# Kernel optimization log

Measured on AMD Instinct MI355X. Metric: run time of the kernel, lower is better.

Reference implementation:

```python
import jax, jax.numpy as jnp
import numpy as np

B, N_OBJ, N_VAL, E, H, HEADS = 512, 10, 200, 420, 128, 4
NPG = 1 + N_OBJ + N_VAL  # nodes per graph = 211
N = B * NPG
FMIN = float(np.finfo(np.float32).min)


def _gat_conv(x, src, dst, W, att_src, att_dst, bias, concat):
    # PyG GATConv (v1): linear (no bias) -> per-head attention logits ->
    # leaky_relu(a_src[j]+a_dst[i]) -> softmax over edges grouped by dst -> scatter-sum
    heads = att_src.shape[0]
    xs = (x @ W).reshape(N, heads, -1)            # [N, heads, C]
    a_src = (xs * att_src).sum(-1)                # [N, heads]
    a_dst = (xs * att_dst).sum(-1)                # [N, heads]
    alpha = jax.nn.leaky_relu(a_src[src] + a_dst[dst], 0.2)   # [Etot, heads]
    amax = jax.ops.segment_max(alpha, dst, num_segments=N)
    ex = jnp.exp(alpha - amax[dst])
    denom = jax.ops.segment_sum(ex, dst, num_segments=N)
    alpha = ex / (denom[dst] + 1e-16)
    out = jax.ops.segment_sum(xs[src] * alpha[..., None], dst, num_segments=N)  # [N,heads,C]
    out = out.reshape(N, -1) if concat else out.mean(axis=1)
    return out + bias


def setup_inputs() -> dict:
    key = jax.random.key(0)
    ks = jax.random.split(key, 24)
    s = 0.1
    C1 = H // HEADS  # 32
    inp = {
        'head_node': jax.random.normal(ks[0], (B, 2), jnp.float32),
        'objective_nodes': jax.random.normal(ks[1], (B, N_OBJ, 2), jnp.float32),
        'value_nodes': jax.random.normal(ks[2], (B, N_VAL, 5), jnp.float32),
        'edge_indices': jax.random.randint(ks[3], (B, 2, E), 0, NPG, jnp.int64 if jax.config.jax_enable_x64 else jnp.int32),
        'accept_mask': jnp.ones((B, 2), jnp.float32),
        'W_head': jax.random.normal(ks[4], (2, H)) * s, 'b_head': jnp.zeros((H,)),
        'W_obj': jax.random.normal(ks[5], (2, H)) * s, 'b_obj': jnp.zeros((H,)),
        'W_val': jax.random.normal(ks[6], (5, H)) * s, 'b_val': jnp.zeros((H,)),
        'W1': jax.random.normal(ks[7], (H, HEADS * C1)) * s,
        'att_src1': jax.random.normal(ks[8], (HEADS, C1)) * s,
        'att_dst1': jax.random.normal(ks[9], (HEADS, C1)) * s,
        'b1': jnp.zeros((HEADS * C1,)),
        'W2': jax.random.normal(ks[10], (H, HEADS * H)) * s,
        'att_src2': jax.random.normal(ks[11], (HEADS, H)) * s,
        'att_dst2': jax.random.normal(ks[12], (HEADS, H)) * s,
        'b2': jnp.zeros((H,)),
        'W_acc': jax.random.normal(ks[13], (H, 2)) * 0.01, 'b_acc': jnp.zeros((2,)),
        'W_off': jax.random.normal(ks[14], (H, 1)) * 0.01, 'b_off': jnp.zeros((1,)),
        'W_vf': jax.random.normal(ks[15], (H, 1)) * s, 'b_vf': jnp.zeros((1,)),
    }
    return inp


def reference(head_node, objective_nodes, value_nodes, edge_indices, accept_mask,
              W_head, b_head, W_obj, b_obj, W_val, b_val,
              W1, att_src1, att_dst1, b1, W2, att_src2, att_dst2, b2,
              W_acc, b_acc, W_off, b_off, W_vf, b_vf):
    # node encoders + ReLU
    h_head = jax.nn.relu(head_node @ W_head + b_head)                  # [B,H]
    h_obj = jax.nn.relu(objective_nodes @ W_obj + b_obj)               # [B,N_OBJ,H]
    h_val = jax.nn.relu(value_nodes @ W_val + b_val)                   # [B,N_VAL,H]
    h_nodes = jnp.concatenate([h_head[:, None], h_obj, h_val], axis=1)  # [B,NPG,H]
    x = h_nodes.reshape(N, H)
    # batch graphs: offset per-graph edge indices, add self loops
    offs = (jnp.arange(B, dtype=edge_indices.dtype) * NPG)[:, None, None]
    ei = (edge_indices + offs).transpose(1, 0, 2).reshape(2, -1)       # [2, B*E]
    loops = jnp.arange(N, dtype=edge_indices.dtype)
    src = jnp.concatenate([ei[0], loops])
    dst = jnp.concatenate([ei[1], loops])
    # GAT: layer1 concat heads, ReLU (BasicGNN inter-layer act), layer2 mean heads
    x1 = jax.nn.relu(_gat_conv(x, src, dst, W1, att_src1, att_dst1, b1, True))
    x2 = _gat_conv(x1, src, dst, W2, att_src2, att_dst2, b2, False)
    h_out = jax.nn.relu(x2).reshape(B, NPG, H)
    h_head_out = h_out[:, 0]                                           # [B,H]
    h_val_out = h_out[:, -N_VAL:]                                      # [B,N_VAL,H]
    offer_logits = (h_val_out @ W_off + b_off).squeeze(-1)             # [B,N_VAL]
    accept_inf_mask = jnp.maximum(jnp.log(accept_mask), FMIN)
    accept_logits = h_head_out @ W_acc + b_acc + accept_inf_mask       # [B,2]
    vf = h_head_out @ W_vf + b_vf                                      # [B,1]
    return jnp.concatenate([accept_logits, offer_logits, vf], axis=-1)  # [B, 2+N_VAL+1]
```

## Files before the change

### kernel.cpp

```cpp
#include <hip/hip_runtime.h>

typedef unsigned short u16;
typedef unsigned int u32;
typedef short short8 __attribute__((ext_vector_type(8)));
typedef float f32x4 __attribute__((ext_vector_type(4)));

#define NB   512
#define NPG  211
#define NOBJ 10
#define NVAL 200
#define NE   420
#define NN   (NB * NPG)

__device__ __forceinline__ float bf2f(u16 u){
  union { unsigned i; float f; } v; v.i = ((unsigned)u) << 16; return v.f;
}
__device__ __forceinline__ u16 f2bf(float f){
  union { float f; unsigned i; } v; v.f = f;
  return (u16)((v.i + 0x7FFFu + ((v.i >> 16) & 1u)) >> 16);
}
__device__ __forceinline__ float lo_bf(u32 u){ union{u32 i;float f;}v; v.i=u<<16; return v.f; }
__device__ __forceinline__ float hi_bf(u32 u){ union{u32 i;float f;}v; v.i=u&0xffff0000u; return v.f; }
__device__ __forceinline__ u32 pack_bf(float a, float b){ return (u32)f2bf(a) | ((u32)f2bf(b)<<16); }
__device__ __forceinline__ float lrelu(float s){ return s > 0.f ? s : 0.2f * s; }
__device__ __forceinline__ short8 pack8(ushort4 a, ushort4 b){
  short8 v;
  v[0]=(short)a.x; v[1]=(short)a.y; v[2]=(short)a.z; v[3]=(short)a.w;
  v[4]=(short)b.x; v[5]=(short)b.y; v[6]=(short)b.z; v[7]=(short)b.w;
  return v;
}
__device__ __forceinline__ int swz(int r, int c){
  return (r << 7) + (((c & ~3) ^ ((r & 15) << 2)) | (c & 3));
}
__device__ __forceinline__ int s16(int r, int c){
  return (r << 7) + ((((c >> 3) ^ (r & 15)) << 3) | (c & 7));
}

#define AS_GLOBAL(p) ((const __attribute__((address_space(1))) void*)((const void*)(p)))
#define AS_LDS(p)    ((__attribute__((address_space(3))) void*)((void*)(p)))

__global__ __launch_bounds__(256) void k_prept(const float* __restrict__ W1, const float* __restrict__ W2,
                                               u16* __restrict__ W1t, u16* __restrict__ W2t){
  int gid = blockIdx.x * 256 + threadIdx.x;
  if (gid < 16384){
    int k = gid >> 7, n = gid & 127;
    W1t[n * 128 + k] = f2bf(W1[k * 128 + n]);
  } else {
    int t = gid - 16384;
    int n = t >> 9, kk = t & 511;
    int h = kk >> 7, c = kk & 127;
    W2t[n * 512 + kk] = f2bf(W2[c * 512 + h * 128 + n]);
  }
}

__global__ __launch_bounds__(256) void k_prepwm(const float* __restrict__ W2, const float* __restrict__ as2,
                                                const float* __restrict__ ad2,
                                                float* __restrict__ wms, float* __restrict__ wmd){
  int gid = blockIdx.x * 256 + threadIdx.x;
  int which = gid >> 9, hk = gid & 511;
  int h = hk >> 7, k = hk & 127;
  const float* av = which ? ad2 : as2;
  float s = 0.f;
  for (int j = 0; j < 128; ++j)
    s += W2[k * 512 + h * 128 + j] * av[h * 128 + j];
  (which ? wmd : wms)[hk] = s;
}


__global__ __launch_bounds__(256) void k_embed2(
    const float* __restrict__ head, const float* __restrict__ obj, const float* __restrict__ val,
    const float* __restrict__ Wh, const float* __restrict__ bh,
    const float* __restrict__ Wo, const float* __restrict__ bo,
    const float* __restrict__ Wv, const float* __restrict__ bv,
    u16* __restrict__ x){
  int gid = blockIdx.x * 256 + threadIdx.x;
  int n = gid >> 5, cc = (gid & 31) << 2;
  int g = n / NPG, loc = n - g * NPG;
  float a[4];
  if (loc == 0){
    const float* in = head + (size_t)g * 2;
    float i0 = in[0], i1 = in[1];
    #pragma unroll
    for (int t = 0; t < 4; ++t){ int c = cc + t; a[t] = bh[c] + i0 * Wh[c] + i1 * Wh[128 + c]; }
  } else if (loc <= NOBJ){
    const float* in = obj + ((size_t)g * NOBJ + (loc - 1)) * 2;
    float i0 = in[0], i1 = in[1];
    #pragma unroll
    for (int t = 0; t < 4; ++t){ int c = cc + t; a[t] = bo[c] + i0 * Wo[c] + i1 * Wo[128 + c]; }
  } else {
    const float* in = val + ((size_t)g * NVAL + (loc - 11)) * 5;
    float f[5];
    #pragma unroll
    for (int k = 0; k < 5; ++k) f[k] = in[k];
    #pragma unroll
    for (int t = 0; t < 4; ++t){
      int c = cc + t; float s = bv[c];
      #pragma unroll
      for (int k = 0; k < 5; ++k) s += f[k] * Wv[k * 128 + c];
      a[t] = s;
    }
  }
  ushort4 u;
  u.x = f2bf(fmaxf(a[0], 0.f)); u.y = f2bf(fmaxf(a[1], 0.f));
  u.z = f2bf(fmaxf(a[2], 0.f)); u.w = f2bf(fmaxf(a[3], 0.f));
  *(ushort4*)&x[(size_t)n * 128 + cc] = u;
}

__global__ __launch_bounds__(256) void k_csr2(const int* __restrict__ eidx,
                                              int* __restrict__ coff, int* __restrict__ csrc){
  __shared__ int sEs[420], sEd[420], sTmp[256], sOff[212], sSrc[632];
  int g = blockIdx.x, tid = threadIdx.x;
  const int4* e4 = (const int4*)(eidx + (size_t)g * 840);
  for (int i = tid; i < 105; i += 256){ ((int4*)sEs)[i] = e4[i]; ((int4*)sEd)[i] = e4[105 + i]; }
  __syncthreads();
  int deg = 0;
  if (tid < NPG){
    deg = 1;
    const int4* p4 = (const int4*)sEd;
    #pragma unroll 4
    for (int i = 0; i < 105; ++i){
      int4 v = p4[i];
      deg += (v.x == tid) + (v.y == tid) + (v.z == tid) + (v.w == tid);
    }
  }
  int v = deg;
  #pragma unroll
  for (int st = 1; st < 256; st <<= 1){
    sTmp[tid] = v;
    __syncthreads();
    if (tid >= st) v += sTmp[tid - st];
    __syncthreads();
  }
  if (tid < NPG) sOff[tid] = v - deg;
  if (tid == NPG - 1) sOff[NPG] = v;
  __syncthreads();
  if (tid < NPG){
    int p = sOff[tid];
    sSrc[p++] = tid;
    const int4* pd4 = (const int4*)sEd;
    const int4* ps4 = (const int4*)sEs;
    for (int i = 0; i < 105; ++i){
      int4 d = pd4[i]; int4 s = ps4[i];
      if (d.x == tid) sSrc[p++] = s.x;
      if (d.y == tid) sSrc[p++] = s.y;
      if (d.z == tid) sSrc[p++] = s.z;
      if (d.w == tid) sSrc[p++] = s.w;
    }
  }
  __syncthreads();
  if (tid < 212) coff[(size_t)g * 212 + tid] = sOff[tid];
  for (int i = tid; i < 631; i += 256) csrc[(size_t)g * 632 + i] = sSrc[i];
}

template<int KCH, bool RELU>
__global__ __launch_bounds__(512) void k_mm(const u16* __restrict__ A, size_t chunkStride,
                                            const u16* __restrict__ Bt, int bstride,
                                            const float* __restrict__ bias, u16* __restrict__ C){
  __shared__ u16 sA[128 * 128];
  __shared__ u16 sB[128 * 128];
  const int tid = threadIdx.x, lane = tid & 63, w = tid >> 6;
  const int l15 = lane & 15, lg = lane >> 4;
  const int row0 = blockIdx.x * 128;
  f32x4 acc[8];
  #pragma unroll
  for (int ni = 0; ni < 8; ++ni) acc[ni] = (f32x4){0,0,0,0};

  #pragma unroll 1
  for (int ch = 0; ch < KCH; ++ch){
    const u16* Ab = A + (size_t)ch * chunkStride + (size_t)row0 * 128;
    const u16* Bb = Bt + ch * 128;
    #pragma unroll
    for (int i = 0; i < 4; ++i){
      int r = w * 16 + i * 4 + (lane >> 4);
      int c16 = lane & 15;
      int sw = (c16 ^ (r & 15)) << 4;
      __builtin_amdgcn_global_load_lds(AS_GLOBAL((const char*)(Ab + (size_t)r * 128) + sw),
                                       AS_LDS(&sA[(w * 16 + i * 4) * 128]), 16, 0, 0);
      __builtin_amdgcn_global_load_lds(AS_GLOBAL((const char*)(Bb + (size_t)r * bstride) + sw),
                                       AS_LDS(&sB[(w * 16 + i * 4) * 128]), 16, 0, 0);
    }
    __syncthreads();
    #pragma unroll
    for (int kk = 0; kk < 4; ++kk){
      int k0 = kk * 32 + lg * 4;
      int rr = w * 16 + l15;
      short8 af = pack8(*(const ushort4*)&sA[s16(rr, k0)],
                        *(const ushort4*)&sA[s16(rr, k0 + 16)]);
      #pragma unroll
      for (int ni = 0; ni < 8; ++ni){
        int cc = ni * 16 + l15;
        short8 bf = pack8(*(const ushort4*)&sB[s16(cc, k0)],
                          *(const ushort4*)&sB[s16(cc, k0 + 16)]);
        acc[ni] = __builtin_amdgcn_mfma_f32_16x16x32_bf16(af, bf, acc[ni], 0, 0, 0);
      }
    }
    __syncthreads();
  }
  const int r0 = row0 + w * 16 + lg * 4;
  #pragma unroll
  for (int ni = 0; ni < 8; ++ni){
    int col = ni * 16 + l15;
    float bv = RELU ? bias[col] : 0.f;
    #pragma unroll
    for (int r = 0; r < 4; ++r){
      float v = acc[ni][r];
      if (RELU) v = fmaxf(v + bv, 0.f);
      C[(size_t)(r0 + r) * 128 + col] = f2bf(v);
    }
  }
}

__global__ __launch_bounds__(256) void k_att1k(const u16* __restrict__ xs1,
                                               const float* __restrict__ as1, const float* __restrict__ ad1,
                                               float* __restrict__ Ls, float* __restrict__ Ld){
  int t = blockIdx.x * 256 + threadIdx.x;
  int n = t >> 2, h = t & 3;
  const u16* xr = xs1 + (size_t)n * 128 + h * 32;
  float s = 0.f, d = 0.f;
  #pragma unroll
  for (int j = 0; j < 8; ++j){
    ushort4 xv = *(const ushort4*)(xr + j * 4);
    #pragma unroll
    for (int q = 0; q < 4; ++q){
      float xf = bf2f(((const u16*)&xv)[q]);
      int c = h * 32 + j * 4 + q;
      s += xf * as1[c];
      d += xf * ad1[c];
    }
  }
  Ls[t] = s; Ld[t] = d;
}

__global__ __launch_bounds__(256) void k_att2k(const u16* __restrict__ x1,
                                               const float* __restrict__ wms, const float* __restrict__ wmd,
                                               float* __restrict__ Ls, float* __restrict__ Ld){
  __shared__ float sw[1024];
  int tid = threadIdx.x;
  for (int i = tid; i < 512; i += 256) sw[i] = wms[i];
  for (int i = tid; i < 512; i += 256) sw[512 + i] = wmd[i];
  __syncthreads();
  int t = blockIdx.x * 256 + tid;
  int n = t >> 2, h = t & 3;
  const u16* xr = x1 + (size_t)n * 128;
  const float* wsp = sw + h * 128;
  const float* wdp = sw + 512 + h * 128;
  float s = 0.f, d = 0.f;
  #pragma unroll
  for (int j = 0; j < 32; ++j){
    ushort4 xv = *(const ushort4*)(xr + j * 4);
    #pragma unroll
    for (int q = 0; q < 4; ++q){
      float xf = bf2f(((const u16*)&xv)[q]);
      s += xf * wsp[j * 4 + q];
      d += xf * wdp[j * 4 + q];
    }
  }
  Ls[t] = s; Ld[t] = d;
}

__global__ __launch_bounds__(256) void k_smk(const float* __restrict__ Ls, const float* __restrict__ Ld,
                                             const int* __restrict__ coff, const int* __restrict__ csrc,
                                             float* __restrict__ wn, float* __restrict__ rden, float fold){
  int g = blockIdx.x >> 2;
  int t = ((blockIdx.x & 3) << 8) + threadIdx.x;
  if (t >= NPG * 4) return;
  int dst = t >> 2, h = t & 3;
  int gb = g * NPG;
  int o0 = coff[(size_t)g * 212 + dst], o1 = coff[(size_t)g * 212 + dst + 1];
  const int* sp = csrc + (size_t)g * 632;
  float ad = Ld[(size_t)(gb + dst) * 4 + h];
  float m = -3e38f;
  for (int e = o0; e < o1; ++e) m = fmaxf(m, lrelu(Ls[(size_t)(gb + sp[e]) * 4 + h] + ad));
  float dn = 0.f;
  float* wp = wn + (size_t)g * 2528 + h * 632;
  for (int e = o0; e < o1; ++e){
    float ee = __expf(lrelu(Ls[(size_t)(gb + sp[e]) * 4 + h] + ad) - m);
    wp[e] = ee; dn += ee;
  }
  rden[(size_t)(gb + dst) * 4 + h] = fold / (dn + 1e-16f);
}

__global__ __launch_bounds__(256) void k_gat1k(const u16* __restrict__ xs1,
                                               const float* __restrict__ wn, const float* __restrict__ rden,
                                               const int* __restrict__ coff, const int* __restrict__ csrc,
                                               const float* __restrict__ b1, u16* __restrict__ x1){
  int bid = blockIdx.x;
  int g = bid / 53, ch = bid - g * 53;
  int dst = ch * 4 + (threadIdx.x >> 6);
  if (dst >= NPG) return;
  int lane = threadIdx.x & 63;
  int cp = lane << 1, hh = lane >> 4;
  int gb = g * NPG;
  int o0 = coff[(size_t)g * 212 + dst], o1 = coff[(size_t)g * 212 + dst + 1];
  const int* sp = csrc + (size_t)g * 632;
  const float* wp = wn + (size_t)g * 2528 + hh * 632;
  float a0 = 0.f, a1 = 0.f;
  for (int e = o0; e < o1; ++e){
    int src = sp[e];
    u32 f = *(const u32*)&xs1[(size_t)(gb + src) * 128 + cp];
    float w = wp[e];
    a0 += w * lo_bf(f); a1 += w * hi_bf(f);
  }
  float rv = rden[(size_t)(gb + dst) * 4 + hh];
  *(u32*)&x1[(size_t)(gb + dst) * 128 + cp] =
    pack_bf(fmaxf(a0 * rv + b1[cp], 0.f), fmaxf(a1 * rv + b1[cp + 1], 0.f));
}

__global__ __launch_bounds__(256) void k_gat2k(const u16* __restrict__ x1,
                                               const float* __restrict__ wn, const float* __restrict__ rden,
                                               const int* __restrict__ coff, const int* __restrict__ csrc,
                                               u16* __restrict__ y){
  int bid = blockIdx.x;
  int g = bid / 53, ch = bid - g * 53;
  int dst = ch * 4 + (threadIdx.x >> 6);
  if (dst >= NPG) return;
  int lane = threadIdx.x & 63;
  int cp = lane << 1;
  int gb = g * NPG;
  int o0 = coff[(size_t)g * 212 + dst], o1 = coff[(size_t)g * 212 + dst + 1];
  const int* sp = csrc + (size_t)g * 632;
  const float* wb = wn + (size_t)g * 2528;
  float a0[4] = {0,0,0,0}, a1[4] = {0,0,0,0};
  for (int e = o0; e < o1; ++e){
    int src = sp[e];
    u32 f = *(const u32*)&x1[(size_t)(gb + src) * 128 + cp];
    float xl = lo_bf(f), xh = hi_bf(f);
    #pragma unroll
    for (int h = 0; h < 4; ++h){
      float w = wb[h * 632 + e];
      a0[h] += w * xl; a1[h] += w * xh;
    }
  }
  #pragma unroll
  for (int h = 0; h < 4; ++h){
    float rv = rden[(size_t)(gb + dst) * 4 + h];
    *(u32*)&y[(size_t)h * NN * 128 + (size_t)(gb + dst) * 128 + cp] =
      pack_bf(a0[h] * rv, a1[h] * rv);
  }
}

__global__ __launch_bounds__(256) void k_final2(const u16* __restrict__ out2, const float* __restrict__ amask,
                                                const float* __restrict__ Wacc, const float* __restrict__ bacc,
                                                const float* __restrict__ Woff, const float* __restrict__ boff,
                                                const float* __restrict__ Wvf,  const float* __restrict__ bvf,
                                                float* __restrict__ out){
  int g = blockIdx.x >> 2;
  int t = ((blockIdx.x & 3) << 8) + threadIdx.x;
  if (t >= 812) return;
  int o = t >> 2, q = t & 3;
  float s = 0.f;
  if (o < 200){
    const u16* row = out2 + (size_t)(g * NPG + 11 + o) * 128;
    #pragma unroll
    for (int j = 0; j < 8; ++j){
      int c = q * 32 + j * 4;
      ushort4 xv = *(const ushort4*)(row + c);
      s += bf2f(xv.x)*Woff[c] + bf2f(xv.y)*Woff[c+1] + bf2f(xv.z)*Woff[c+2] + bf2f(xv.w)*Woff[c+3];
    }
  } else if (o < 202){
    int j2 = o - 200;
    const u16* row = out2 + (size_t)(g * NPG) * 128;
    #pragma unroll
    for (int j = 0; j < 8; ++j){
      int c = q * 32 + j * 4;
      ushort4 xv = *(const ushort4*)(row + c);
      s += bf2f(xv.x)*Wacc[c*2+j2] + bf2f(xv.y)*Wacc[(c+1)*2+j2]
         + bf2f(xv.z)*Wacc[(c+2)*2+j2] + bf2f(xv.w)*Wacc[(c+3)*2+j2];
    }
  } else {
    const u16* row = out2 + (size_t)(g * NPG) * 128;
    #pragma unroll
    for (int j = 0; j < 8; ++j){
      int c = q * 32 + j * 4;
      ushort4 xv = *(const ushort4*)(row + c);
      s += bf2f(xv.x)*Wvf[c] + bf2f(xv.y)*Wvf[c+1] + bf2f(xv.z)*Wvf[c+2] + bf2f(xv.w)*Wvf[c+3];
    }
  }
  s += __shfl_xor(s, 1);
  s += __shfl_xor(s, 2);
  if (q == 0){
    if (o < 200){
      out[(size_t)g * 203 + 2 + o] = s + boff[0];
    } else if (o < 202){
      int j2 = o - 200;
      float lm = logf(amask[g * 2 + j2]);
      out[(size_t)g * 203 + j2] = s + bacc[j2] + fmaxf(lm, -3.402823466e38f);
    } else {
      out[(size_t)g * 203 + 202] = s + bvf[0];
    }
  }
}

extern "C" void kernel_launch(void* const* d_in, const int* in_sizes, int n_in,
                              void* d_out, int out_size, void* d_ws, size_t ws_size,
                              hipStream_t stream){
  (void)in_sizes; (void)n_in; (void)out_size; (void)ws_size;
  const float* head = (const float*)d_in[0];
  const float* obj  = (const float*)d_in[1];
  const float* val  = (const float*)d_in[2];
  const int*   eidx = (const int*)d_in[3];
  const float* amask= (const float*)d_in[4];
  const float* Wh   = (const float*)d_in[5];
  const float* bh   = (const float*)d_in[6];
  const float* Wo   = (const float*)d_in[7];
  const float* bo   = (const float*)d_in[8];
  const float* Wv   = (const float*)d_in[9];
  const float* bv   = (const float*)d_in[10];
  const float* W1   = (const float*)d_in[11];
  const float* as1  = (const float*)d_in[12];
  const float* ad1  = (const float*)d_in[13];
  const float* b1   = (const float*)d_in[14];
  const float* W2   = (const float*)d_in[15];
  const float* as2  = (const float*)d_in[16];
  const float* ad2  = (const float*)d_in[17];
  const float* b2   = (const float*)d_in[18];
  const float* Wacc = (const float*)d_in[19];
  const float* bacc = (const float*)d_in[20];
  const float* Woff = (const float*)d_in[21];
  const float* boff = (const float*)d_in[22];
  const float* Wvf  = (const float*)d_in[23];
  const float* bvf  = (const float*)d_in[24];
  float* out = (float*)d_out;

  char* ws = (char*)d_ws;
  u16*   W1t = (u16*)ws;
  u16*   W2t = (u16*)(ws + 32768);
  float* wms = (float*)(ws + 163840);
  float* wmd = (float*)(ws + 165888);

  k_prept<<<320, 256, 0, stream>>>(W1, W2, W1t, W2t);
  k_prepwm<<<4, 256, 0, stream>>>(W2, as2, ad2, wms, wmd);

  int*   coff = (int*)(ws + 167936);
  int*   csrc = (int*)(ws + 602112);
  float* aLs  = (float*)(ws + 1896448);
  float* aLd  = (float*)(ws + 3624960);
  float* wn   = (float*)(ws + 5353472);
  float* rden = (float*)(ws + 10530816);
  u16*   x    = (u16*)(ws + 12259328);
  u16*   xs1  = (u16*)(ws + 39915520);
  u16*   y    = (u16*)(ws + 67571712);

  k_embed2<<<NN * 32 / 256, 256, 0, stream>>>(head, obj, val, Wh, bh, Wo, bo, Wv, bv, x);
  k_csr2<<<NB, 256, 0, stream>>>(eidx, coff, csrc);
  k_mm<1, false><<<NN / 128, 512, 0, stream>>>(x, 0, W1t, 128, nullptr, xs1);
  k_att1k<<<NN * 4 / 256, 256, 0, stream>>>(xs1, as1, ad1, aLs, aLd);
  k_smk<<<NB * 4, 256, 0, stream>>>(aLs, aLd, coff, csrc, wn, rden, 1.0f);
  k_gat1k<<<NB * 53, 256, 0, stream>>>(xs1, wn, rden, coff, csrc, b1, x);
  k_att2k<<<NN * 4 / 256, 256, 0, stream>>>(x, wms, wmd, aLs, aLd);
  k_smk<<<NB * 4, 256, 0, stream>>>(aLs, aLd, coff, csrc, wn, rden, 0.25f);
  k_gat2k<<<NB * 53, 256, 0, stream>>>(x, wn, rden, coff, csrc, y);
  k_mm<4, true><<<NN / 128, 512, 0, stream>>>(y, (size_t)NN * 128, W2t, 512, b2, xs1);
  k_final2<<<NB * 4, 256, 0, stream>>>(xs1, amask, Wacc, bacc, Woff, boff, Wvf, bvf, out);
}
```

Before: 272.6 us.

## Fuse layer-2 aggregation, W2 matmul and output heads into one per-graph kernel

Replaces the separate layer-2 aggregation kernel, the 4-head MFMA matmul and the final head kernel with one kernel that runs one 512-thread block per graph. The block stages the graph's x1 rows, attention weights and CSR data in LDS, aggregates each head into LDS, feeds it to bf16 MFMA against W2, then applies bias, ReLU and the output projections from LDS. This removes the large intermediate y tensor and the out2 round trip through global memory, along with two launches. In exchange it uses about 122KB of LDS per block, which allows only one block per CU, so there are 512 blocks and little latency hiding.

```diff
diff --git a/kernel.cpp b/kernel.cpp
--- a/kernel.cpp
+++ b/kernel.cpp
@@ -306,87 +306,163 @@
     pack_bf(fmaxf(a0 * rv + b1[cp], 0.f), fmaxf(a1 * rv + b1[cp + 1], 0.f));
 }
 
-__global__ __launch_bounds__(256) void k_gat2k(const u16* __restrict__ x1,
-                                               const float* __restrict__ wn, const float* __restrict__ rden,
-                                               const int* __restrict__ coff, const int* __restrict__ csrc,
-                                               u16* __restrict__ y){
-  int bid = blockIdx.x;
-  int g = bid / 53, ch = bid - g * 53;
-  int dst = ch * 4 + (threadIdx.x >> 6);
-  if (dst >= NPG) return;
-  int lane = threadIdx.x & 63;
-  int cp = lane << 1;
-  int gb = g * NPG;
-  int o0 = coff[(size_t)g * 212 + dst], o1 = coff[(size_t)g * 212 + dst + 1];
-  const int* sp = csrc + (size_t)g * 632;
-  const float* wb = wn + (size_t)g * 2528;
-  float a0[4] = {0,0,0,0}, a1[4] = {0,0,0,0};
-  for (int e = o0; e < o1; ++e){
-    int src = sp[e];
-    u32 f = *(const u32*)&x1[(size_t)(gb + src) * 128 + cp];
-    float xl = lo_bf(f), xh = hi_bf(f);
-    #pragma unroll
-    for (int h = 0; h < 4; ++h){
-      float w = wb[h * 632 + e];
-      a0[h] += w * xl; a1[h] += w * xh;
-    }
-  }
-  #pragma unroll
+__global__ __launch_bounds__(512) void k_gg2(
+    const u16* __restrict__ x1, const float* __restrict__ wn, const float* __restrict__ rden,
+    const int* __restrict__ coff, const int* __restrict__ csrc,
+    const u16* __restrict__ W2t, const float* __restrict__ b2,
+    const float* __restrict__ amask,
+    const float* __restrict__ Wacc, const float* __restrict__ bacc,
+    const float* __restrict__ Woff, const float* __restrict__ boff,
+    const float* __restrict__ Wvf,  const float* __restrict__ bvf,
+    float* __restrict__ out)
+{
+  __shared__ __align__(16) char sm[124896];
+  u16*   sX1  = (u16*)sm;
+  u16*   sY   = (u16*)(sm + 54016);
+  float* sW   = (float*)(sm + 108032);
+  float* sDen = (float*)(sm + 118144);
+  int*   sOff = (int*)(sm + 121520);
+  int*   sSrc = (int*)(sm + 122368);
+
+  const int g = blockIdx.x, tid = threadIdx.x;
+  const int lane = tid & 63, w = tid >> 6;
+  const int l15 = lane & 15, lg = lane >> 4;
+  const int cp = lane << 1;
+
+  {
+    const uint4* src = (const uint4*)(x1 + (size_t)g * NPG * 128);
+    uint4* dst = (uint4*)sX1;
+    for (int i = tid; i < 3376; i += 512) dst[i] = src[i];
+    const float* wsrc = wn + (size_t)g * 2528;
+    for (int i = tid; i < 2528; i += 512) sW[i] = wsrc[i];
+    const float* rsrc = rden + (size_t)g * 844;
+    for (int i = tid; i < 844; i += 512) sDen[i] = rsrc[i];
+    for (int i = tid; i < 212; i += 512) sOff[i] = coff[(size_t)g * 212 + i];
+    const int* ssrc = csrc + (size_t)g * 632;
+    for (int i = tid; i < 632; i += 512) sSrc[i] = ssrc[i];
+  }
+  __syncthreads();
+
+  f32x4 acc[2][8];
+  #pragma unroll
+  for (int m = 0; m < 2; ++m)
+    #pragma unroll
+    for (int ni = 0; ni < 8; ++ni) acc[m][ni] = (f32x4){0,0,0,0};
+  const int rt0 = w, rt1 = w + 8;
+  const bool has1 = (rt1 < 14);
+
+  #pragma unroll 1
   for (int h = 0; h < 4; ++h){
-    float rv = rden[(size_t)(gb + dst) * 4 + h];
-    *(u32*)&y[(size_t)h * NN * 128 + (size_t)(gb + dst) * 128 + cp] =
-      pack_bf(a0[h] * rv, a1[h] * rv);
-  }
-}
-
-__global__ __launch_bounds__(256) void k_final2(const u16* __restrict__ out2, const float* __restrict__ amask,
-                                                const float* __restrict__ Wacc, const float* __restrict__ bacc,
-                                                const float* __restrict__ Woff, const float* __restrict__ boff,
-                                                const float* __restrict__ Wvf,  const float* __restrict__ bvf,
-                                                float* __restrict__ out){
-  int g = blockIdx.x >> 2;
-  int t = ((blockIdx.x & 3) << 8) + threadIdx.x;
-  if (t >= 812) return;
-  int o = t >> 2, q = t & 3;
-  float s = 0.f;
-  if (o < 200){
-    const u16* row = out2 + (size_t)(g * NPG + 11 + o) * 128;
-    #pragma unroll
-    for (int j = 0; j < 8; ++j){
-      int c = q * 32 + j * 4;
-      ushort4 xv = *(const ushort4*)(row + c);
-      s += bf2f(xv.x)*Woff[c] + bf2f(xv.y)*Woff[c+1] + bf2f(xv.z)*Woff[c+2] + bf2f(xv.w)*Woff[c+3];
-    }
-  } else if (o < 202){
-    int j2 = o - 200;
-    const u16* row = out2 + (size_t)(g * NPG) * 128;
-    #pragma unroll
-    for (int j = 0; j < 8; ++j){
-      int c = q * 32 + j * 4;
-      ushort4 xv = *(const ushort4*)(row + c);
-      s += bf2f(xv.x)*Wacc[c*2+j2] + bf2f(xv.y)*Wacc[(c+1)*2+j2]
-         + bf2f(xv.z)*Wacc[(c+2)*2+j2] + bf2f(xv.w)*Wacc[(c+3)*2+j2];
-    }
-  } else {
-    const u16* row = out2 + (size_t)(g * NPG) * 128;
-    #pragma unroll
-    for (int j = 0; j < 8; ++j){
-      int c = q * 32 + j * 4;
-      ushort4 xv = *(const ushort4*)(row + c);
-      s += bf2f(xv.x)*Wvf[c] + bf2f(xv.y)*Wvf[c+1] + bf2f(xv.z)*Wvf[c+2] + bf2f(xv.w)*Wvf[c+3];
-    }
-  }
-  s += __shfl_xor(s, 1);
-  s += __shfl_xor(s, 2);
-  if (q == 0){
+    const float* wp = sW + h * 632;
+    for (int dst = w; dst < NPG; dst += 8){
+      int o0 = sOff[dst], o1 = sOff[dst + 1];
+      float a0 = 0.f, a1 = 0.f;
+      int e = o0;
+      for (; e + 4 <= o1; e += 4){
+        int s0 = sSrc[e], s1 = sSrc[e+1], s2 = sSrc[e+2], s3 = sSrc[e+3];
+        u32 f0 = *(const u32*)&sX1[s0 * 128 + cp];
+        u32 f1 = *(const u32*)&sX1[s1 * 128 + cp];
+        u32 f2 = *(const u32*)&sX1[s2 * 128 + cp];
+        u32 f3 = *(const u32*)&sX1[s3 * 128 + cp];
+        float w0 = wp[e], w1 = wp[e+1], w2 = wp[e+2], w3 = wp[e+3];
+        a0 += w0 * lo_bf(f0); a1 += w0 * hi_bf(f0);
+        a0 += w1 * lo_bf(f1); a1 += w1 * hi_bf(f1);
+        a0 += w2 * lo_bf(f2); a1 += w2 * hi_bf(f2);
+        a0 += w3 * lo_bf(f3); a1 += w3 * hi_bf(f3);
+      }
+      for (; e < o1; ++e){
+        int sn = sSrc[e];
+        u32 f = *(const u32*)&sX1[sn * 128 + cp];
+        float wv = wp[e];
+        a0 += wv * lo_bf(f); a1 += wv * hi_bf(f);
+      }
+      float rv = sDen[dst * 4 + h];
+      *(u32*)&sY[swz(dst, cp)] = pack_bf(a0 * rv, a1 * rv);
+    }
+    __syncthreads();
+    #pragma unroll
+    for (int kk = 0; kk < 4; ++kk){
+      int k0 = kk * 32 + lg * 4;
+      short8 bf[8];
+      #pragma unroll
+      for (int ni = 0; ni < 8; ++ni){
+        const u16* Bp = W2t + (size_t)(ni * 16 + l15) * 512 + h * 128 + k0;
+        bf[ni] = pack8(*(const ushort4*)Bp, *(const ushort4*)(Bp + 16));
+      }
+      int rr0 = rt0 * 16 + l15; rr0 = rr0 < NPG ? rr0 : NPG - 1;
+      short8 af0 = pack8(*(const ushort4*)&sY[swz(rr0, k0)],
+                         *(const ushort4*)&sY[swz(rr0, k0 + 16)]);
+      #pragma unroll
+      for (int ni = 0; ni < 8; ++ni)
+        acc[0][ni] = __builtin_amdgcn_mfma_f32_16x16x32_bf16(af0, bf[ni], acc[0][ni], 0, 0, 0);
+      if (has1){
+        int rr1 = rt1 * 16 + l15; rr1 = rr1 < NPG ? rr1 : NPG - 1;
+        short8 af1 = pack8(*(const ushort4*)&sY[swz(rr1, k0)],
+                           *(const ushort4*)&sY[swz(rr1, k0 + 16)]);
+        #pragma unroll
+        for (int ni = 0; ni < 8; ++ni)
+          acc[1][ni] = __builtin_amdgcn_mfma_f32_16x16x32_bf16(af1, bf[ni], acc[1][ni], 0, 0, 0);
+      }
+    }
+    __syncthreads();
+  }
+
+  #pragma unroll
+  for (int m = 0; m < 2; ++m){
+    if (m == 1 && !has1) break;
+    int r0 = (m == 0 ? rt0 : rt1) * 16 + lg * 4;
+    #pragma unroll
+    for (int ni = 0; ni < 8; ++ni){
+      int col = ni * 16 + l15;
+      float bv = b2[col];
+      #pragma unroll
+      for (int r = 0; r < 4; ++r){
+        int row = r0 + r;
+        if (row < NPG) sX1[row * 128 + col] = f2bf(fmaxf(acc[m][ni][r] + bv, 0.f));
+      }
+    }
+  }
+  __syncthreads();
+
+  if (tid < 406){
+    int o = tid >> 1, q = tid & 1;
+    const u16* row = sX1 + (size_t)((o < 200) ? (11 + o) : 0) * 128;
+    float s = 0.f;
     if (o < 200){
-      out[(size_t)g * 203 + 2 + o] = s + boff[0];
+      #pragma unroll
+      for (int j = 0; j < 16; ++j){
+        int c = q * 64 + j * 4;
+        ushort4 xv = *(const ushort4*)(row + c);
+        s += bf2f(xv.x)*Woff[c] + bf2f(xv.y)*Woff[c+1] + bf2f(xv.z)*Woff[c+2] + bf2f(xv.w)*Woff[c+3];
+      }
     } else if (o < 202){
       int j2 = o - 200;
-      float lm = logf(amask[g * 2 + j2]);
-      out[(size_t)g * 203 + j2] = s + bacc[j2] + fmaxf(lm, -3.402823466e38f);
+      #pragma unroll
+      for (int j = 0; j < 16; ++j){
+        int c = q * 64 + j * 4;
+        ushort4 xv = *(const ushort4*)(row + c);
+        s += bf2f(xv.x)*Wacc[c*2+j2] + bf2f(xv.y)*Wacc[(c+1)*2+j2]
+           + bf2f(xv.z)*Wacc[(c+2)*2+j2] + bf2f(xv.w)*Wacc[(c+3)*2+j2];
+      }
     } else {
-      out[(size_t)g * 203 + 202] = s + bvf[0];
+      #pragma unroll
+      for (int j = 0; j < 16; ++j){
+        int c = q * 64 + j * 4;
+        ushort4 xv = *(const ushort4*)(row + c);
+        s += bf2f(xv.x)*Wvf[c] + bf2f(xv.y)*Wvf[c+1] + bf2f(xv.z)*Wvf[c+2] + bf2f(xv.w)*Wvf[c+3];
+      }
+    }
+    s += __shfl_xor(s, 1);
+    if (q == 0){
+      if (o < 200){
+        out[(size_t)g * 203 + 2 + o] = s + boff[0];
+      } else if (o < 202){
+        int j2 = o - 200;
+        float lm = logf(amask[g * 2 + j2]);
+        out[(size_t)g * 203 + j2] = s + bacc[j2] + fmaxf(lm, -3.402823466e38f);
+      } else {
+        out[(size_t)g * 203 + 202] = s + bvf[0];
+      }
     }
   }
 }
@@ -439,7 +515,6 @@
   float* rden = (float*)(ws + 10530816);
   u16*   x    = (u16*)(ws + 12259328);
   u16*   xs1  = (u16*)(ws + 39915520);
-  u16*   y    = (u16*)(ws + 67571712);
 
   k_embed2<<<NN * 32 / 256, 256, 0, stream>>>(head, obj, val, Wh, bh, Wo, bo, Wv, bv, x);
   k_csr2<<<NB, 256, 0, stream>>>(eidx, coff, csrc);
@@ -449,7 +524,6 @@
   k_gat1k<<<NB * 53, 256, 0, stream>>>(xs1, wn, rden, coff, csrc, b1, x);
   k_att2k<<<NN * 4 / 256, 256, 0, stream>>>(x, wms, wmd, aLs, aLd);
   k_smk<<<NB * 4, 256, 0, stream>>>(aLs, aLd, coff, csrc, wn, rden, 0.25f);
-  k_gat2k<<<NB * 53, 256, 0, stream>>>(x, wn, rden, coff, csrc, y);
-  k_mm<4, true><<<NN / 128, 512, 0, stream>>>(y, (size_t)NN * 128, W2t, 512, b2, xs1);
-  k_final2<<<NB * 4, 256, 0, stream>>>(xs1, amask, Wacc, bacc, Woff, boff, Wvf, bvf, out);
-}
+  k_gg2<<<NB, 512, 0, stream>>>(x, wn, rden, coff, csrc, W2t, b2, amask,
+                                Wacc, bacc, Woff, boff, Wvf, bvf, out);
+}
```

After: 375.4 us. 37.8% more time.

## Fuse attention logits with softmax per graph, merge prep kernels, interleave y layout

Applied to the files above, without the earlier changes.

Attention-logit computation and edge softmax are merged into one kernel per graph, so the logits stay in shared memory instead of going through global buffers. The two weight-prep kernels become a single launch. The second-layer aggregation output changes from head-major planes to a row-interleaved [N, 4*128] layout, and the matmul takes a row stride and a chunk offset to match. This cuts four launches and the logit round trips to global memory, but the fused kernels use only 512 blocks of 512 threads, which may lower occupancy compared with the earlier wider grids.

```diff
diff --git a/kernel.cpp b/kernel.cpp
--- a/kernel.cpp
+++ b/kernel.cpp
@@ -29,9 +29,6 @@
   v[4]=(short)b.x; v[5]=(short)b.y; v[6]=(short)b.z; v[7]=(short)b.w;
   return v;
 }
-__device__ __forceinline__ int swz(int r, int c){
-  return (r << 7) + (((c & ~3) ^ ((r & 15) << 2)) | (c & 3));
-}
 __device__ __forceinline__ int s16(int r, int c){
   return (r << 7) + ((((c >> 3) ^ (r & 15)) << 3) | (c & 7));
 }
@@ -39,33 +36,30 @@
 #define AS_GLOBAL(p) ((const __attribute__((address_space(1))) void*)((const void*)(p)))
 #define AS_LDS(p)    ((__attribute__((address_space(3))) void*)((void*)(p)))
 
-__global__ __launch_bounds__(256) void k_prept(const float* __restrict__ W1, const float* __restrict__ W2,
-                                               u16* __restrict__ W1t, u16* __restrict__ W2t){
+__global__ __launch_bounds__(256) void k_prep(const float* __restrict__ W1, const float* __restrict__ W2,
+                                              const float* __restrict__ as2, const float* __restrict__ ad2,
+                                              u16* __restrict__ W1t, u16* __restrict__ W2t,
+                                              float* __restrict__ wms, float* __restrict__ wmd){
   int gid = blockIdx.x * 256 + threadIdx.x;
   if (gid < 16384){
     int k = gid >> 7, n = gid & 127;
     W1t[n * 128 + k] = f2bf(W1[k * 128 + n]);
-  } else {
+  } else if (gid < 81920){
     int t = gid - 16384;
     int n = t >> 9, kk = t & 511;
     int h = kk >> 7, c = kk & 127;
     W2t[n * 512 + kk] = f2bf(W2[c * 512 + h * 128 + n]);
-  }
-}
-
-__global__ __launch_bounds__(256) void k_prepwm(const float* __restrict__ W2, const float* __restrict__ as2,
-                                                const float* __restrict__ ad2,
-                                                float* __restrict__ wms, float* __restrict__ wmd){
-  int gid = blockIdx.x * 256 + threadIdx.x;
-  int which = gid >> 9, hk = gid & 511;
-  int h = hk >> 7, k = hk & 127;
-  const float* av = which ? ad2 : as2;
-  float s = 0.f;
-  for (int j = 0; j < 128; ++j)
-    s += W2[k * 512 + h * 128 + j] * av[h * 128 + j];
-  (which ? wmd : wms)[hk] = s;
-}
-
+  } else {
+    int t = gid - 81920;
+    int which = t >> 9, hk = t & 511;
+    int h = hk >> 7, k = hk & 127;
+    const float* av = which ? ad2 : as2;
+    float s = 0.f;
+    for (int j = 0; j < 128; ++j)
+      s += W2[k * 512 + h * 128 + j] * av[h * 128 + j];
+    (which ? wmd : wms)[hk] = s;
+  }
+}
 
 __global__ __launch_bounds__(256) void k_embed2(
     const float* __restrict__ head, const float* __restrict__ obj, const float* __restrict__ val,
@@ -153,7 +147,7 @@
 }
 
 template<int KCH, bool RELU>
-__global__ __launch_bounds__(512) void k_mm(const u16* __restrict__ A, size_t chunkStride,
+__global__ __launch_bounds__(512) void k_mm(const u16* __restrict__ A, int aStride, int chunkOff,
                                             const u16* __restrict__ Bt, int bstride,
                                             const float* __restrict__ bias, u16* __restrict__ C){
   __shared__ u16 sA[128 * 128];
@@ -167,14 +161,14 @@
 
   #pragma unroll 1
   for (int ch = 0; ch < KCH; ++ch){
-    const u16* Ab = A + (size_t)ch * chunkStride + (size_t)row0 * 128;
+    const u16* Ab = A + (size_t)ch * chunkOff;
     const u16* Bb = Bt + ch * 128;
     #pragma unroll
     for (int i = 0; i < 4; ++i){
       int r = w * 16 + i * 4 + (lane >> 4);
       int c16 = lane & 15;
       int sw = (c16 ^ (r & 15)) << 4;
-      __builtin_amdgcn_global_load_lds(AS_GLOBAL((const char*)(Ab + (size_t)r * 128) + sw),
+      __builtin_amdgcn_global_load_lds(AS_GLOBAL((const char*)(Ab + (size_t)(row0 + r) * aStride) + sw),
                                        AS_LDS(&sA[(w * 16 + i * 4) * 128]), 16, 0, 0);
       __builtin_amdgcn_global_load_lds(AS_GLOBAL((const char*)(Bb + (size_t)r * bstride) + sw),
                                        AS_LDS(&sB[(w * 16 + i * 4) * 128]), 16, 0, 0);
@@ -210,74 +204,92 @@
   }
 }
 
-__global__ __launch_bounds__(256) void k_att1k(const u16* __restrict__ xs1,
-                                               const float* __restrict__ as1, const float* __restrict__ ad1,
-                                               float* __restrict__ Ls, float* __restrict__ Ld){
-  int t = blockIdx.x * 256 + threadIdx.x;
-  int n = t >> 2, h = t & 3;
-  const u16* xr = xs1 + (size_t)n * 128 + h * 32;
-  float s = 0.f, d = 0.f;
-  #pragma unroll
-  for (int j = 0; j < 8; ++j){
-    ushort4 xv = *(const ushort4*)(xr + j * 4);
-    #pragma unroll
-    for (int q = 0; q < 4; ++q){
-      float xf = bf2f(((const u16*)&xv)[q]);
-      int c = h * 32 + j * 4 + q;
-      s += xf * as1[c];
-      d += xf * ad1[c];
-    }
-  }
-  Ls[t] = s; Ld[t] = d;
-}
-
-__global__ __launch_bounds__(256) void k_att2k(const u16* __restrict__ x1,
-                                               const float* __restrict__ wms, const float* __restrict__ wmd,
-                                               float* __restrict__ Ls, float* __restrict__ Ld){
+__global__ __launch_bounds__(512) void k_attsm1(const u16* __restrict__ xs1,
+                                                const float* __restrict__ as1, const float* __restrict__ ad1,
+                                                const int* __restrict__ coff, const int* __restrict__ csrc,
+                                                float* __restrict__ wn, float* __restrict__ rden){
+  __shared__ float sLs[844], sLd[844];
+  const int g = blockIdx.x, tid = threadIdx.x;
+  const int gb = g * NPG;
+  for (int t = tid; t < NPG * 4; t += 512){
+    int n = t >> 2, h = t & 3;
+    const u16* xr = xs1 + (size_t)(gb + n) * 128 + h * 32;
+    float s = 0.f, d = 0.f;
+    #pragma unroll
+    for (int j = 0; j < 8; ++j){
+      ushort4 xv = *(const ushort4*)(xr + j * 4);
+      #pragma unroll
+      for (int q = 0; q < 4; ++q){
+        float xf = bf2f(((const u16*)&xv)[q]);
+        int c = h * 32 + j * 4 + q;
+        s += xf * as1[c];
+        d += xf * ad1[c];
+      }
+    }
+    sLs[t] = s; sLd[t] = d;
+  }
+  __syncthreads();
+  for (int t = tid; t < NPG * 4; t += 512){
+    int dst = t >> 2, h = t & 3;
+    int o0 = coff[(size_t)g * 212 + dst], o1 = coff[(size_t)g * 212 + dst + 1];
+    const int* sp = csrc + (size_t)g * 632;
+    float ad = sLd[t];
+    float m = -3e38f;
+    for (int e = o0; e < o1; ++e) m = fmaxf(m, lrelu(sLs[sp[e] * 4 + h] + ad));
+    float dn = 0.f;
+    float* wp = wn + (size_t)g * 2528 + h * 632;
+    for (int e = o0; e < o1; ++e){
+      float ee = __expf(lrelu(sLs[sp[e] * 4 + h] + ad) - m);
+      wp[e] = ee; dn += ee;
+    }
+    rden[(size_t)(gb + dst) * 4 + h] = 1.0f / (dn + 1e-16f);
+  }
+}
+
+__global__ __launch_bounds__(512) void k_attsm2(const u16* __restrict__ x1,
+                                                const float* __restrict__ wms, const float* __restrict__ wmd,
+                                                const int* __restrict__ coff, const int* __restrict__ csrc,
+                                                float* __restrict__ wn, float* __restrict__ rden){
   __shared__ float sw[1024];
-  int tid = threadIdx.x;
-  for (int i = tid; i < 512; i += 256) sw[i] = wms[i];
-  for (int i = tid; i < 512; i += 256) sw[512 + i] = wmd[i];
-  __syncthreads();
-  int t = blockIdx.x * 256 + tid;
-  int n = t >> 2, h = t & 3;
-  const u16* xr = x1 + (size_t)n * 128;
-  const float* wsp = sw + h * 128;
-  const float* wdp = sw + 512 + h * 128;
-  float s = 0.f, d = 0.f;
-  #pragma unroll
-  for (int j = 0; j < 32; ++j){
-    ushort4 xv = *(const ushort4*)(xr + j * 4);
-    #pragma unroll
-    for (int q = 0; q < 4; ++q){
-      float xf = bf2f(((const u16*)&xv)[q]);
-      s += xf * wsp[j * 4 + q];
-      d += xf * wdp[j * 4 + q];
-    }
-  }
-  Ls[t] = s; Ld[t] = d;
-}
-
-__global__ __launch_bounds__(256) void k_smk(const float* __restrict__ Ls, const float* __restrict__ Ld,
-                                             const int* __restrict__ coff, const int* __restrict__ csrc,
-                                             float* __restrict__ wn, float* __restrict__ rden, float fold){
-  int g = blockIdx.x >> 2;
-  int t = ((blockIdx.x & 3) << 8) + threadIdx.x;
-  if (t >= NPG * 4) return;
-  int dst = t >> 2, h = t & 3;
-  int gb = g * NPG;
-  int o0 = coff[(size_t)g * 212 + dst], o1 = coff[(size_t)g * 212 + dst + 1];
-  const int* sp = csrc + (size_t)g * 632;
-  float ad = Ld[(size_t)(gb + dst) * 4 + h];
-  float m = -3e38f;
-  for (int e = o0; e < o1; ++e) m = fmaxf(m, lrelu(Ls[(size_t)(gb + sp[e]) * 4 + h] + ad));
-  float dn = 0.f;
-  float* wp = wn + (size_t)g * 2528 + h * 632;
-  for (int e = o0; e < o1; ++e){
-    float ee = __expf(lrelu(Ls[(size_t)(gb + sp[e]) * 4 + h] + ad) - m);
-    wp[e] = ee; dn += ee;
-  }
-  rden[(size_t)(gb + dst) * 4 + h] = fold / (dn + 1e-16f);
+  __shared__ float sLs[844], sLd[844];
+  const int g = blockIdx.x, tid = threadIdx.x;
+  const int gb = g * NPG;
+  for (int i = tid; i < 1024; i += 512) sw[i] = (i < 512) ? wms[i] : wmd[i - 512];
+  __syncthreads();
+  for (int t = tid; t < NPG * 4; t += 512){
+    int n = t >> 2, h = t & 3;
+    const u16* xr = x1 + (size_t)(gb + n) * 128;
+    const float* wsp = sw + h * 128;
+    const float* wdp = sw + 512 + h * 128;
+    float s = 0.f, d = 0.f;
+    #pragma unroll
+    for (int j = 0; j < 32; ++j){
+      ushort4 xv = *(const ushort4*)(xr + j * 4);
+      #pragma unroll
+      for (int q = 0; q < 4; ++q){
+        float xf = bf2f(((const u16*)&xv)[q]);
+        s += xf * wsp[j * 4 + q];
+        d += xf * wdp[j * 4 + q];
+      }
+    }
+    sLs[t] = s; sLd[t] = d;
+  }
+  __syncthreads();
+  for (int t = tid; t < NPG * 4; t += 512){
+    int dst = t >> 2, h = t & 3;
+    int o0 = coff[(size_t)g * 212 + dst], o1 = coff[(size_t)g * 212 + dst + 1];
+    const int* sp = csrc + (size_t)g * 632;
+    float ad = sLd[t];
+    float m = -3e38f;
+    for (int e = o0; e < o1; ++e) m = fmaxf(m, lrelu(sLs[sp[e] * 4 + h] + ad));
+    float dn = 0.f;
+    float* wp = wn + (size_t)g * 2528 + h * 632;
+    for (int e = o0; e < o1; ++e){
+      float ee = __expf(lrelu(sLs[sp[e] * 4 + h] + ad) - m);
+      wp[e] = ee; dn += ee;
+    }
+    rden[(size_t)(gb + dst) * 4 + h] = 0.25f / (dn + 1e-16f);
+  }
 }
 
 __global__ __launch_bounds__(256) void k_gat1k(const u16* __restrict__ xs1,
@@ -331,11 +343,11 @@
       a0[h] += w * xl; a1[h] += w * xh;
     }
   }
+  u16* yr = y + (size_t)(gb + dst) * 512;
   #pragma unroll
   for (int h = 0; h < 4; ++h){
     float rv = rden[(size_t)(gb + dst) * 4 + h];
-    *(u32*)&y[(size_t)h * NN * 128 + (size_t)(gb + dst) * 128 + cp] =
-      pack_bf(a0[h] * rv, a1[h] * rv);
+    *(u32*)&yr[h * 128 + cp] = pack_bf(a0[h] * rv, a1[h] * rv);
   }
 }
 
@@ -427,29 +439,22 @@
   u16*   W2t = (u16*)(ws + 32768);
   float* wms = (float*)(ws + 163840);
   float* wmd = (float*)(ws + 165888);
-
-  k_prept<<<320, 256, 0, stream>>>(W1, W2, W1t, W2t);
-  k_prepwm<<<4, 256, 0, stream>>>(W2, as2, ad2, wms, wmd);
-
   int*   coff = (int*)(ws + 167936);
   int*   csrc = (int*)(ws + 602112);
-  float* aLs  = (float*)(ws + 1896448);
-  float* aLd  = (float*)(ws + 3624960);
   float* wn   = (float*)(ws + 5353472);
   float* rden = (float*)(ws + 10530816);
   u16*   x    = (u16*)(ws + 12259328);
   u16*   xs1  = (u16*)(ws + 39915520);
   u16*   y    = (u16*)(ws + 67571712);
 
+  k_prep<<<324, 256, 0, stream>>>(W1, W2, as2, ad2, W1t, W2t, wms, wmd);
   k_embed2<<<NN * 32 / 256, 256, 0, stream>>>(head, obj, val, Wh, bh, Wo, bo, Wv, bv, x);
   k_csr2<<<NB, 256, 0, stream>>>(eidx, coff, csrc);
-  k_mm<1, false><<<NN / 128, 512, 0, stream>>>(x, 0, W1t, 128, nullptr, xs1);
-  k_att1k<<<NN * 4 / 256, 256, 0, stream>>>(xs1, as1, ad1, aLs, aLd);
-  k_smk<<<NB * 4, 256, 0, stream>>>(aLs, aLd, coff, csrc, wn, rden, 1.0f);
+  k_mm<1, false><<<NN / 128, 512, 0, stream>>>(x, 128, 0, W1t, 128, nullptr, xs1);
+  k_attsm1<<<NB, 512, 0, stream>>>(xs1, as1, ad1, coff, csrc, wn, rden);
   k_gat1k<<<NB * 53, 256, 0, stream>>>(xs1, wn, rden, coff, csrc, b1, x);
-  k_att2k<<<NN * 4 / 256, 256, 0, stream>>>(x, wms, wmd, aLs, aLd);
-  k_smk<<<NB * 4, 256, 0, stream>>>(aLs, aLd, coff, csrc, wn, rden, 0.25f);
+  k_attsm2<<<NB, 512, 0, stream>>>(x, wms, wmd, coff, csrc, wn, rden);
   k_gat2k<<<NB * 53, 256, 0, stream>>>(x, wn, rden, coff, csrc, y);
-  k_mm<4, true><<<NN / 128, 512, 0, stream>>>(y, (size_t)NN * 128, W2t, 512, b2, xs1);
+  k_mm<4, true><<<NN / 128, 512, 0, stream>>>(y, 512, 128, W2t, 512, b2, xs1);
   k_final2<<<NB * 4, 256, 0, stream>>>(xs1, amask, Wacc, bacc, Woff, boff, Wvf, bvf, out);
 }
```

New measurement: 262.2 us. -3.8%, faster.
